# Optimization experiments

Hardware: AMD Instinct MI355X
Metric: run time of the kernel (lower is better)

Reference implementation:

```python
import jax, jax.numpy as jnp
import numpy as np

H = 64  # hidden_size

def _xavier(key, shape):
    fan_in, fan_out = shape[1], shape[0]
    limit = float(np.sqrt(6.0 / (fan_in + fan_out)))
    return jax.random.uniform(key, shape, jnp.float32, -limit, limit)

def setup_inputs() -> dict:
    key = jax.random.key(0)
    ks = jax.random.split(key, 4)
    B, T, I = 4096, 512, 1
    x = jax.random.normal(ks[0], (B, T, I), jnp.float32)
    W_ih = _xavier(ks[1], (H, I))      # input->hidden
    W_hh = _xavier(ks[2], (H, H))      # hidden->hidden
    b_ih = jnp.zeros((H,), jnp.float32)
    b_hh = jnp.zeros((H,), jnp.float32)
    fc_w = _xavier(ks[3], (1, H))      # final linear
    fc_b = jnp.zeros((1,), jnp.float32)
    return {"x": x, "W_ih": W_ih, "W_hh": W_hh, "b_ih": b_ih,
            "b_hh": b_hh, "fc_w": fc_w, "fc_b": fc_b}

def reference(x, W_ih, W_hh, b_ih, b_hh, fc_w, fc_b):
    # Precompute input projection for all timesteps: [B, T, H]
    xw = jnp.einsum('bti,hi->bth', x, W_ih) + b_ih
    h0 = jnp.zeros((x.shape[0], H), x.dtype)

    def step(h, xw_t):
        h = jnp.tanh(xw_t + h @ W_hh.T + b_hh)
        return h, None

    # scan over time (axis 0 after transpose): sequential recurrence
    h_last, _ = jax.lax.scan(step, h0, jnp.swapaxes(xw, 0, 1))
    return h_last @ fc_w.T + fc_b  # [B, 1]
```

## Files before the change

kernel.cpp:

```cpp
#include <hip/hip_runtime.h>
#include <stdint.h>

#define HDIM 64
#define TDIM 512
#define GB   16


typedef float    f32x4 __attribute__((ext_vector_type(4)));
typedef _Float16 f16x8 __attribute__((ext_vector_type(8)));
typedef _Float16 f16x2 __attribute__((ext_vector_type(2)));
typedef unsigned int u32;
typedef unsigned int u32x2 __attribute__((ext_vector_type(2)));
typedef unsigned int u32x4 __attribute__((ext_vector_type(4)));

__device__ __forceinline__ u32 pk2(float a, float b) {
    return __builtin_bit_cast(u32, __builtin_amdgcn_cvt_pkrtz(a, b));
}
__device__ __forceinline__ float hi_mask(float v) {
    return __builtin_bit_cast(float, __builtin_bit_cast(u32, v) & 0xFFFFE000u);
}

__global__ __launch_bounds__(256, 1)
__attribute__((amdgpu_waves_per_eu(1)))
void rnn_quadwave(const float* __restrict__ x,
                  const float* __restrict__ W_ih,
                  const float* __restrict__ W_hh,
                  const float* __restrict__ b_ih,
                  const float* __restrict__ b_hh,
                  const float* __restrict__ fc_w,
                  const float* __restrict__ fc_b,
                  float* __restrict__ out,
                  int B)
{
    __shared__ __align__(16) u32 st[4][64][4];
    __shared__ float xs[64][GB];
    __shared__ float red[4][GB];

    const int tid  = threadIdx.x;
    const int lane = tid & 63;
    const int w    = tid >> 6;
    const int b    = lane & 15;
    const int g    = lane >> 4;
    const int m16  = lane & 15;
    const int gb0  = blockIdx.x * GB;
    const int wc   = w >> 1;
    const int wh   = w & 1;

    const float K = 2.885390081777927f;

    f16x8 Ahi0, Ahi1, Alo0, Alo1;
    {
        const int wr = 32*wc + 8*(m16 >> 2) + 4*wh + (m16 & 3);
        const float* wrow = W_hh + wr * HDIM;
        const f32x4 va0 = *(const f32x4*)(wrow + 8*g);
        const f32x4 vb0 = *(const f32x4*)(wrow + 8*g + 4);
        const f32x4 va1 = *(const f32x4*)(wrow + 32 + 8*g);
        const f32x4 vb1 = *(const f32x4*)(wrow + 32 + 8*g + 4);
#pragma unroll
        for (int e = 0; e < 4; ++e) {
            float v; _Float16 h;
            v = K*va0[e]; h = (_Float16)v; Ahi0[e]   = h; Alo0[e]   = (_Float16)(v - (float)h);
            v = K*vb0[e]; h = (_Float16)v; Ahi0[e+4] = h; Alo0[e+4] = (_Float16)(v - (float)h);
            v = K*va1[e]; h = (_Float16)v; Ahi1[e]   = h; Alo1[e]   = (_Float16)(v - (float)h);
            v = K*vb1[e]; h = (_Float16)v; Ahi1[e+4] = h; Alo1[e+4] = (_Float16)(v - (float)h);
        }
    }

    float wihc[4], biasc[4];
#pragma unroll
    for (int r = 0; r < 4; ++r) {
        const int idx = 32*wc + 8*g + 4*wh + r;
        wihc[r]  = K * W_ih[idx];
        biasc[r] = K * (b_ih[idx] + b_hh[idx]);
    }

    {
        const u32x4 z = {0u, 0u, 0u, 0u};
        ((u32x4*)st)[tid] = z;
    }

    const int sm = tid >> 4;
    const int tq = tid & 15;
    const f32x4 zero4 = {0.f, 0.f, 0.f, 0.f};

    float hv0 = 0.f, hv1 = 0.f, hv2 = 0.f, hv3 = 0.f;

#pragma unroll 1
    for (int tc = 0; tc < TDIM/64; ++tc) {
        const f32x4 xv4 = *(const f32x4*)(x + (size_t)(gb0 + sm) * TDIM
                                            + tc*64 + tq*4);
        xs[tq*4 + 0][sm] = xv4.x;
        xs[tq*4 + 1][sm] = xv4.y;
        xs[tq*4 + 2][sm] = xv4.z;
        xs[tq*4 + 3][sm] = xv4.w;
        __syncthreads();

#pragma unroll 1
        for (int tj = 0; tj < 64; ++tj) {
            const f16x8 ih0 = __builtin_bit_cast(f16x8, *(const u32x4*)&st[0][lane][0]);
            const f16x8 ih1 = __builtin_bit_cast(f16x8, *(const u32x4*)&st[1][lane][0]);
            const f16x8 il0 = __builtin_bit_cast(f16x8, *(const u32x4*)&st[2][lane][0]);
            const f16x8 il1 = __builtin_bit_cast(f16x8, *(const u32x4*)&st[3][lane][0]);
            const float xt = xs[tj][b];

            f32x4 c1, c2, c3;
            c1.x = fmaf(xt, wihc[0], biasc[0]);
            c1.y = fmaf(xt, wihc[1], biasc[1]);
            c1.z = fmaf(xt, wihc[2], biasc[2]);
            c1.w = fmaf(xt, wihc[3], biasc[3]);
            c2 = zero4; c3 = zero4;

            c1 = __builtin_amdgcn_mfma_f32_16x16x32_f16(Ahi0, ih0, c1, 0, 0, 0);
            c2 = __builtin_amdgcn_mfma_f32_16x16x32_f16(Ahi0, il0, c2, 0, 0, 0);
            c3 = __builtin_amdgcn_mfma_f32_16x16x32_f16(Alo0, ih0, c3, 0, 0, 0);
            c1 = __builtin_amdgcn_mfma_f32_16x16x32_f16(Ahi1, ih1, c1, 0, 0, 0);
            c2 = __builtin_amdgcn_mfma_f32_16x16x32_f16(Ahi1, il1, c2, 0, 0, 0);
            c3 = __builtin_amdgcn_mfma_f32_16x16x32_f16(Alo1, ih1, c3, 0, 0, 0);

            const float z0 = c1.x + (c2.x + c3.x);
            const float z1 = c1.y + (c2.y + c3.y);
            const float z2 = c1.z + (c2.z + c3.z);
            const float z3 = c1.w + (c2.w + c3.w);
            hv0 = fmaf(-2.0f, __builtin_amdgcn_rcpf(__builtin_amdgcn_exp2f(z0) + 1.0f), 1.0f);
            hv1 = fmaf(-2.0f, __builtin_amdgcn_rcpf(__builtin_amdgcn_exp2f(z1) + 1.0f), 1.0f);
            hv2 = fmaf(-2.0f, __builtin_amdgcn_rcpf(__builtin_amdgcn_exp2f(z2) + 1.0f), 1.0f);
            hv3 = fmaf(-2.0f, __builtin_amdgcn_rcpf(__builtin_amdgcn_exp2f(z3) + 1.0f), 1.0f);

            const float h0 = hi_mask(hv0), h1 = hi_mask(hv1);
            const float h2 = hi_mask(hv2), h3 = hi_mask(hv3);
            u32x2 nh, nl;
            nh.x = pk2(h0, h1);           nh.y = pk2(h2, h3);
            nl.x = pk2(hv0-h0, hv1-h1);   nl.y = pk2(hv2-h2, hv3-h3);

            __syncthreads();
            *(u32x2*)&st[wc][lane][2*wh]   = nh;
            *(u32x2*)&st[2+wc][lane][2*wh] = nl;
            __syncthreads();
        }
    }

    float acc = 0.0f;
    acc = fmaf(hv0, fc_w[32*wc + 8*g + 4*wh + 0], acc);
    acc = fmaf(hv1, fc_w[32*wc + 8*g + 4*wh + 1], acc);
    acc = fmaf(hv2, fc_w[32*wc + 8*g + 4*wh + 2], acc);
    acc = fmaf(hv3, fc_w[32*wc + 8*g + 4*wh + 3], acc);
    acc += __shfl_xor(acc, 16, 64);
    acc += __shfl_xor(acc, 32, 64);
    if (lane < 16) red[w][lane] = acc;
    __syncthreads();
    if (tid < GB)
        out[gb0 + tid] = red[0][tid] + red[1][tid] + red[2][tid] + red[3][tid]
                       + fc_b[0];
}

extern "C" void kernel_launch(void* const* d_in, const int* in_sizes, int n_in,
                              void* d_out, int out_size, void* d_ws, size_t ws_size,
                              hipStream_t stream)
{
    const float* x    = (const float*)d_in[0];
    const float* W_ih = (const float*)d_in[1];
    const float* W_hh = (const float*)d_in[2];
    const float* b_ih = (const float*)d_in[3];
    const float* b_hh = (const float*)d_in[4];
    const float* fc_w = (const float*)d_in[5];
    const float* fc_b = (const float*)d_in[6];
    float* out = (float*)d_out;

    const int B = in_sizes[0] / TDIM;
    const int blocks = B / GB;

    rnn_quadwave<<<blocks, 256, 0, stream>>>(
        x, W_ih, W_hh, b_ih, b_hh, fc_w, fc_b, out, B);
}
```

Measured before the change: 259.2 us.

## Double-buffer hidden state in LDS and split MFMA accumulator chains

The hidden-state staging buffer in shared memory becomes two ping-pong buffers. Each step reads one buffer and writes the other, so the barrier that guarded write-after-read inside each timestep is removed and only one barrier per step remains. The three dependent two-MFMA chains become six independent MFMAs whose results are summed afterwards, which shortens the dependent path through the matrix unit. The cost is twice the shared memory for the state and a few extra vector adds per step.

```diff
diff --git a/kernel.cpp b/kernel.cpp
--- a/kernel.cpp
+++ b/kernel.cpp
@@ -22,7 +22,7 @@
 
 __global__ __launch_bounds__(256, 1)
 __attribute__((amdgpu_waves_per_eu(1)))
-void rnn_quadwave(const float* __restrict__ x,
+void rnn_pingpong(const float* __restrict__ x,
                   const float* __restrict__ W_ih,
                   const float* __restrict__ W_hh,
                   const float* __restrict__ b_ih,
@@ -32,7 +32,7 @@
                   float* __restrict__ out,
                   int B)
 {
-    __shared__ __align__(16) u32 st[4][64][4];
+    __shared__ __align__(16) u32 st[2][4][64][4];
     __shared__ float xs[64][GB];
     __shared__ float red[4][GB];
 
@@ -76,7 +76,8 @@
 
     {
         const u32x4 z = {0u, 0u, 0u, 0u};
-        ((u32x4*)st)[tid] = z;
+        ((u32x4*)st)[tid]       = z;
+        ((u32x4*)st)[tid + 256] = z;
     }
 
     const int sm = tid >> 4;
@@ -97,34 +98,33 @@
 
 #pragma unroll 1
         for (int tj = 0; tj < 64; ++tj) {
-            const f16x8 ih0 = __builtin_bit_cast(f16x8, *(const u32x4*)&st[0][lane][0]);
-            const f16x8 ih1 = __builtin_bit_cast(f16x8, *(const u32x4*)&st[1][lane][0]);
-            const f16x8 il0 = __builtin_bit_cast(f16x8, *(const u32x4*)&st[2][lane][0]);
-            const f16x8 il1 = __builtin_bit_cast(f16x8, *(const u32x4*)&st[3][lane][0]);
+            const int pp = tj & 1;
+            const f16x8 ih0 = __builtin_bit_cast(f16x8, *(const u32x4*)&st[pp][0][lane][0]);
+            const f16x8 ih1 = __builtin_bit_cast(f16x8, *(const u32x4*)&st[pp][1][lane][0]);
+            const f16x8 il0 = __builtin_bit_cast(f16x8, *(const u32x4*)&st[pp][2][lane][0]);
+            const f16x8 il1 = __builtin_bit_cast(f16x8, *(const u32x4*)&st[pp][3][lane][0]);
             const float xt = xs[tj][b];
 
-            f32x4 c1, c2, c3;
+            f32x4 c1, c1b, c2, c2b, c3, c3b;
             c1.x = fmaf(xt, wihc[0], biasc[0]);
             c1.y = fmaf(xt, wihc[1], biasc[1]);
             c1.z = fmaf(xt, wihc[2], biasc[2]);
             c1.w = fmaf(xt, wihc[3], biasc[3]);
-            c2 = zero4; c3 = zero4;
+            c1b = zero4; c2 = zero4; c2b = zero4; c3 = zero4; c3b = zero4;
 
-            c1 = __builtin_amdgcn_mfma_f32_16x16x32_f16(Ahi0, ih0, c1, 0, 0, 0);
-            c2 = __builtin_amdgcn_mfma_f32_16x16x32_f16(Ahi0, il0, c2, 0, 0, 0);
-            c3 = __builtin_amdgcn_mfma_f32_16x16x32_f16(Alo0, ih0, c3, 0, 0, 0);
-            c1 = __builtin_amdgcn_mfma_f32_16x16x32_f16(Ahi1, ih1, c1, 0, 0, 0);
-            c2 = __builtin_amdgcn_mfma_f32_16x16x32_f16(Ahi1, il1, c2, 0, 0, 0);
-            c3 = __builtin_amdgcn_mfma_f32_16x16x32_f16(Alo1, ih1, c3, 0, 0, 0);
+            c1  = __builtin_amdgcn_mfma_f32_16x16x32_f16(Ahi0, ih0, c1,  0, 0, 0);
+            c1b = __builtin_amdgcn_mfma_f32_16x16x32_f16(Ahi1, ih1, c1b, 0, 0, 0);
+            c2  = __builtin_amdgcn_mfma_f32_16x16x32_f16(Ahi0, il0, c2,  0, 0, 0);
+            c2b = __builtin_amdgcn_mfma_f32_16x16x32_f16(Ahi1, il1, c2b, 0, 0, 0);
+            c3  = __builtin_amdgcn_mfma_f32_16x16x32_f16(Alo0, ih0, c3,  0, 0, 0);
+            c3b = __builtin_amdgcn_mfma_f32_16x16x32_f16(Alo1, ih1, c3b, 0, 0, 0);
 
-            const float z0 = c1.x + (c2.x + c3.x);
-            const float z1 = c1.y + (c2.y + c3.y);
-            const float z2 = c1.z + (c2.z + c3.z);
-            const float z3 = c1.w + (c2.w + c3.w);
-            hv0 = fmaf(-2.0f, __builtin_amdgcn_rcpf(__builtin_amdgcn_exp2f(z0) + 1.0f), 1.0f);
-            hv1 = fmaf(-2.0f, __builtin_amdgcn_rcpf(__builtin_amdgcn_exp2f(z1) + 1.0f), 1.0f);
-            hv2 = fmaf(-2.0f, __builtin_amdgcn_rcpf(__builtin_amdgcn_exp2f(z2) + 1.0f), 1.0f);
-            hv3 = fmaf(-2.0f, __builtin_amdgcn_rcpf(__builtin_amdgcn_exp2f(z3) + 1.0f), 1.0f);
+            const f32x4 zsum = (c1 + c1b) + ((c2 + c2b) + (c3 + c3b));
+
+            hv0 = fmaf(-2.0f, __builtin_amdgcn_rcpf(__builtin_amdgcn_exp2f(zsum.x) + 1.0f), 1.0f);
+            hv1 = fmaf(-2.0f, __builtin_amdgcn_rcpf(__builtin_amdgcn_exp2f(zsum.y) + 1.0f), 1.0f);
+            hv2 = fmaf(-2.0f, __builtin_amdgcn_rcpf(__builtin_amdgcn_exp2f(zsum.z) + 1.0f), 1.0f);
+            hv3 = fmaf(-2.0f, __builtin_amdgcn_rcpf(__builtin_amdgcn_exp2f(zsum.w) + 1.0f), 1.0f);
 
             const float h0 = hi_mask(hv0), h1 = hi_mask(hv1);
             const float h2 = hi_mask(hv2), h3 = hi_mask(hv3);
@@ -132,9 +132,8 @@
             nh.x = pk2(h0, h1);           nh.y = pk2(h2, h3);
             nl.x = pk2(hv0-h0, hv1-h1);   nl.y = pk2(hv2-h2, hv3-h3);
 
-            __syncthreads();
-            *(u32x2*)&st[wc][lane][2*wh]   = nh;
-            *(u32x2*)&st[2+wc][lane][2*wh] = nl;
+            *(u32x2*)&st[pp ^ 1][wc][lane][2*wh]     = nh;
+            *(u32x2*)&st[pp ^ 1][2 + wc][lane][2*wh] = nl;
             __syncthreads();
         }
     }
@@ -169,6 +168,6 @@
     const int B = in_sizes[0] / TDIM;
     const int blocks = B / GB;
 
-    rnn_quadwave<<<blocks, 256, 0, stream>>>(
+    rnn_pingpong<<<blocks, 256, 0, stream>>>(
         x, W_ih, W_hh, b_ih, b_hh, fc_w, fc_b, out, B);
 }
```

Measured after the change: 226.5 us. -12.6%, faster.
